# Kernel optimization log

Measured on AMD Instinct MI355X. Metric: run time of the kernel, lower is better.

The kernel has to match this reference:

```python
import jax, jax.numpy as jnp
import numpy as np

E = 8        # num_experts
TOPK = 2     # num_experts_per_tok
D = 1024     # n_embd
H = 2816     # grok FFN hidden dim (multiple_of-rounded 2/3*4*D)
B, T = 4, 2048
COEFF = 0.01 # moe_aux_loss_coeff


def setup_inputs() -> dict:
    key = jax.random.key(0)
    ks = jax.random.split(key, 8)
    s = 0.02  # weight scale so activations stay well-conditioned
    return {
        "x": jax.random.normal(ks[0], (B, T, D), jnp.float32),
        "gate_w": jax.random.normal(ks[1], (D, E), jnp.float32) * s,
        "expert_gate": jax.random.normal(ks[2], (E, D, H), jnp.float32) * s,
        "expert_up": jax.random.normal(ks[3], (E, D, H), jnp.float32) * s,
        "expert_down": jax.random.normal(ks[4], (E, H, D), jnp.float32) * s,
        "shared_gate": jax.random.normal(ks[5], (D, H), jnp.float32) * s,
        "shared_up": jax.random.normal(ks[6], (D, H), jnp.float32) * s,
        "shared_down": jax.random.normal(ks[7], (H, D), jnp.float32) * s,
    }


def _grok_ffn(x, g, u, d):
    # down(gelu(gate(x)) * up(x)); torch F.gelu default = exact erf gelu
    return (jax.nn.gelu(x @ g, approximate=False) * (x @ u)) @ d


def reference(x, gate_w, expert_gate, expert_up, expert_down,
              shared_gate, shared_up, shared_down):
    Bb, Tt, Dd = x.shape
    N = Bb * Tt
    xf = x.reshape(N, Dd)

    # --- router ---
    logits = (xf @ gate_w).astype(jnp.float32)            # (N, E)
    top_logits, top_idx = jax.lax.top_k(logits, TOPK)     # (N, K)
    top_w = jax.nn.softmax(top_logits, axis=-1)           # (N, K)
    gates = jax.nn.softmax(logits, axis=-1)               # (N, E)
    f = jnp.mean(jax.nn.one_hot(top_idx[:, 0], E, dtype=jnp.float32), axis=0)
    P = gates.mean(axis=0)
    aux_loss = COEFF * E * jnp.sum(f * P)

    # dense combine weights (N, E): 0 for unassigned experts
    comb = jnp.zeros((N, E), xf.dtype).at[
        jnp.arange(N)[:, None], top_idx].add(top_w.astype(xf.dtype))

    # --- experts: loop over small fixed E, weight-masked dense FFN ---
    out = jnp.zeros_like(xf)
    for e in range(E):
        ye = _grok_ffn(xf, expert_gate[e], expert_up[e], expert_down[e])
        out = out + comb[:, e:e + 1] * ye

    out = out.reshape(Bb, Tt, Dd)
    out = out + _grok_ffn(xf, shared_gate, shared_up, shared_down).reshape(Bb, Tt, Dd)
    return out, aux_loss
```

## Files before the change

### kernel.cpp

```cpp
#include <hip/hip_runtime.h>
#include <hip/hip_bf16.h>

#define NTOK 8192
#define DIM  1024
#define HID  2816
#define ROWS_CAP 25600
#define TCAP 200

typedef __bf16 bf16x8 __attribute__((ext_vector_type(8)));
typedef float  f32x4  __attribute__((ext_vector_type(4)));

__device__ __forceinline__ unsigned short f2bf(float f) {
  unsigned int x = __float_as_uint(f);
  unsigned int r = (x + 0x7fffu + ((x >> 16) & 1u)) >> 16;
  return (unsigned short)r;
}
__device__ __forceinline__ float gelu_erf(float g) {
  return 0.5f * g * (1.0f + erff(g * 0.70710678118654752f));
}

__device__ __forceinline__ void gload16(const void* g, void* l) {
  __builtin_amdgcn_global_load_lds(
      (__attribute__((address_space(1))) void*)(g),
      (__attribute__((address_space(3))) void*)(l), 16, 0, 0);
}

__device__ __forceinline__ void transpose64(const float* __restrict__ in,
                                            unsigned short* __restrict__ out,
                                            int R, int C) {
  __shared__ float t[64][65];
  int c0 = blockIdx.x * 64, r0 = blockIdx.y * 64;
  int tid = threadIdx.x;
  int lr = tid >> 4;
  int lc4 = (tid & 15) * 4;
  #pragma unroll
  for (int it = 0; it < 4; ++it) {
    int row = lr + it * 16;
    float4 v = *(const float4*)(in + (size_t)(r0 + row) * C + c0 + lc4);
    t[row][lc4] = v.x; t[row][lc4 + 1] = v.y;
    t[row][lc4 + 2] = v.z; t[row][lc4 + 3] = v.w;
  }
  __syncthreads();
  #pragma unroll
  for (int it = 0; it < 4; ++it) {
    int cloc = lr + it * 16;
    ushort4 w = make_ushort4(f2bf(t[lc4][cloc]), f2bf(t[lc4 + 1][cloc]),
                             f2bf(t[lc4 + 2][cloc]), f2bf(t[lc4 + 3][cloc]));
    *(ushort4*)(out + (size_t)(c0 + cloc) * R + r0 + lc4) = w;
  }
}

__global__ __launch_bounds__(256) void k_transpose_DH(
    const float* __restrict__ eg, const float* __restrict__ eu,
    const float* __restrict__ sg, const float* __restrict__ su,
    unsigned short* __restrict__ WgT, unsigned short* __restrict__ WuT,
    unsigned short* __restrict__ SgT, unsigned short* __restrict__ SuT) {
  int z = blockIdx.z;
  const float* in; unsigned short* out;
  if (z < 8)        { in = eg + (size_t)z * DIM * HID;       out = WgT + (size_t)z * DIM * HID; }
  else if (z < 16)  { in = eu + (size_t)(z - 8) * DIM * HID; out = WuT + (size_t)(z - 8) * DIM * HID; }
  else if (z == 16) { in = sg; out = SgT; }
  else              { in = su; out = SuT; }
  transpose64(in, out, DIM, HID);
}

__global__ __launch_bounds__(256) void k_transpose_HD(
    const float* __restrict__ ed, const float* __restrict__ sd,
    unsigned short* __restrict__ WdT, unsigned short* __restrict__ SdT) {
  int z = blockIdx.z;
  const float* in; unsigned short* out;
  if (z < 8) { in = ed + (size_t)z * HID * DIM; out = WdT + (size_t)z * HID * DIM; }
  else       { in = sd; out = SdT; }
  transpose64(in, out, HID, DIM);
}


__global__ __launch_bounds__(256) void k_router(const float* __restrict__ x,
                                                const float* __restrict__ gw,
                                                unsigned short* __restrict__ xb,
                                                int* __restrict__ top_idx,
                                                float* __restrict__ top_w,
                                                int* __restrict__ counts,
                                                float* __restrict__ f_cnt,
                                                float* __restrict__ P_sum) {
  __shared__ float s_p[8];
  __shared__ int   s_cnt[8];
  __shared__ int   s_f[8];
  int tid = threadIdx.x;
  if (tid < 8) { s_p[tid] = 0.f; s_cnt[tid] = 0; s_f[tid] = 0; }
  __syncthreads();

  int lane = tid & 63, wv = tid >> 6;
  float ploc[8] = {0,0,0,0,0,0,0,0};
  int   cloc[8] = {0,0,0,0,0,0,0,0};
  int   floc[8] = {0,0,0,0,0,0,0,0};

  for (int t = blockIdx.x * 4 + wv; t < NTOK; t += 2048) {
    const float4* xr = (const float4*)(x + (size_t)t * DIM) + lane * 4;
    float4 v0 = xr[0], v1 = xr[1], v2 = xr[2], v3 = xr[3];
    float xv[16] = {v0.x, v0.y, v0.z, v0.w, v1.x, v1.y, v1.z, v1.w,
                    v2.x, v2.y, v2.z, v2.w, v3.x, v3.y, v3.z, v3.w};
    ushort4* xw = (ushort4*)(xb + (size_t)t * DIM + lane * 16);
    #pragma unroll
    for (int q = 0; q < 4; ++q)
      xw[q] = make_ushort4(f2bf(xv[q * 4]), f2bf(xv[q * 4 + 1]),
                           f2bf(xv[q * 4 + 2]), f2bf(xv[q * 4 + 3]));
    float acc[8] = {0.f,0.f,0.f,0.f,0.f,0.f,0.f,0.f};
    #pragma unroll
    for (int i = 0; i < 16; ++i) {
      const float* g = gw + (size_t)(lane * 16 + i) * 8;
      #pragma unroll
      for (int e = 0; e < 8; ++e) acc[e] += xv[i] * g[e];
    }
    #pragma unroll
    for (int e = 0; e < 8; ++e) {
      #pragma unroll
      for (int off = 32; off > 0; off >>= 1)
        acc[e] += __shfl_xor(acc[e], off, 64);
    }
    if (lane == 0) {
      int i1 = 0; float l1 = acc[0];
      #pragma unroll
      for (int e = 1; e < 8; ++e) if (acc[e] > l1) { l1 = acc[e]; i1 = e; }
      int i2 = -1; float l2 = -3.0e38f;
      #pragma unroll
      for (int e = 0; e < 8; ++e) if (e != i1 && acc[e] > l2) { l2 = acc[e]; i2 = e; }
      float e2 = expf(l2 - l1);
      float inv12 = 1.0f / (1.0f + e2);
      top_idx[2 * t] = i1; top_idx[2 * t + 1] = i2;
      top_w[2 * t] = inv12; top_w[2 * t + 1] = e2 * inv12;
      float s = 0.f, p[8];
      #pragma unroll
      for (int e = 0; e < 8; ++e) { p[e] = expf(acc[e] - l1); s += p[e]; }
      float invs = 1.0f / s;
      #pragma unroll
      for (int e = 0; e < 8; ++e) {
        ploc[e] += p[e] * invs;
        cloc[e] += (e == i1) + (e == i2);
        floc[e] += (e == i1);
      }
    }
  }
  if (lane == 0) {
    #pragma unroll
    for (int e = 0; e < 8; ++e) {
      atomicAdd(&s_p[e], ploc[e]);
      atomicAdd(&s_cnt[e], cloc[e]);
      atomicAdd(&s_f[e], floc[e]);
    }
  }
  __syncthreads();
  if (tid < 8) {
    atomicAdd(&P_sum[tid], s_p[tid]);
    atomicAdd(&counts[tid], s_cnt[tid]);
    atomicAdd(&f_cnt[tid], (float)s_f[tid]);
  }
}


__global__ __launch_bounds__(256) void k_setup(const int* __restrict__ counts,
                                               int* __restrict__ cursors,
                                               int* __restrict__ tile_expert,
                                               int* __restrict__ tile_row0,
                                               int* __restrict__ perm,
                                               float* __restrict__ wrow) {
  int t = threadIdx.x;
  for (int r = t; r < ROWS_CAP; r += 256) {
    perm[r] = (r < NTOK) ? r : 0;
    wrow[r] = (r < NTOK) ? 1.0f : 0.0f;
  }
  if (t == 0) {
    int so[8], pe[8];
    int cur = NTOK;
    for (int e = 0; e < 8; ++e) {
      so[e] = cur;
      pe[e] = ((counts[e] + 127) >> 7) << 7;
      cur += pe[e];
    }
    for (int e = 0; e < 8; ++e) cursors[e] = so[e];
    for (int tile = 0; tile < TCAP; ++tile) {
      int r0 = tile << 7;
      int ex;
      if (tile < NTOK / 128) ex = 8;
      else if (r0 < cur) {
        ex = 0;
        for (int e = 0; e < 8; ++e) if (r0 >= so[e] && r0 < so[e] + pe[e]) ex = e;
      } else ex = -1;
      tile_expert[tile] = ex;
      tile_row0[tile] = r0;
    }
  }
}

__global__ __launch_bounds__(256) void k_scatter(const int* __restrict__ top_idx,
                                                 const float* __restrict__ top_w,
                                                 int* __restrict__ cursors,
                                                 int* __restrict__ perm,
                                                 float* __restrict__ wrow) {
  int i = blockIdx.x * 256 + threadIdx.x;
  if (i < NTOK * 2) {
    int e = top_idx[i];
    float w = top_w[i];
    int slot = atomicAdd(&cursors[e], 1);
    perm[slot] = i >> 1;
    wrow[slot] = w;
  }
}


__global__ __launch_bounds__(256) void k_stageA(const unsigned short* __restrict__ xb,
    const unsigned short* __restrict__ WgT, const unsigned short* __restrict__ WuT,
    const unsigned short* __restrict__ SgT, const unsigned short* __restrict__ SuT,
    const int* __restrict__ perm,
    const int* __restrict__ tile_expert, const int* __restrict__ tile_row0,
    unsigned short* __restrict__ h, int t0, int row_base) {
  int tile = t0 + blockIdx.y;
  int e = tile_expert[tile];
  if (e < 0) return;
  const unsigned short* Bg = (e < 8) ? WgT + (size_t)e * HID * DIM : SgT;
  const unsigned short* Bu = (e < 8) ? WuT + (size_t)e * HID * DIM : SuT;
  int rows0 = tile_row0[tile];
  int h0 = blockIdx.x * 64;

  __shared__ unsigned short As[2][128 * 64];
  __shared__ unsigned short Bgs[2][64 * 64];
  __shared__ unsigned short Bus[2][64 * 64];

  int tid = threadIdx.x, lane = tid & 63, wv = tid >> 6;
  int wr = wv >> 1, wc = wv & 1;
  int rlo = lane >> 3;
  int koff = (((lane & 7) ^ rlo) * 8);
  int rsw = (lane & 7) << 4;

  int prow[4];
  #pragma unroll
  for (int i = 0; i < 4; ++i) prow[i] = perm[rows0 + i * 32 + wv * 8 + rlo];
  int bn[2];
  #pragma unroll
  for (int i = 0; i < 2; ++i) bn[i] = h0 + i * 32 + wv * 8 + rlo;

  f32x4 accg[4][2] = {};
  f32x4 accu[4][2] = {};

  auto stage = [&](int b, int k0) {
    #pragma unroll
    for (int i = 0; i < 4; ++i)
      gload16(xb + (size_t)prow[i] * DIM + k0 + koff, (char*)As[b] + (i * 32 + wv * 8) * 128);
    #pragma unroll
    for (int i = 0; i < 2; ++i) {
      gload16(Bg + (size_t)bn[i] * DIM + k0 + koff, (char*)Bgs[b] + (i * 32 + wv * 8) * 128);
      gload16(Bu + (size_t)bn[i] * DIM + k0 + koff, (char*)Bus[b] + (i * 32 + wv * 8) * 128);
    }
  };

  auto compute = [&](int b) {
    #pragma unroll
    for (int kk = 0; kk < 2; ++kk) {
      int kbyte = (kk * 64 + (lane >> 4) * 16) ^ rsw;
      bf16x8 a[4], bg[2], bu[2];
      #pragma unroll
      for (int mi = 0; mi < 4; ++mi)
        a[mi] = *(const bf16x8*)((const char*)As[b] + (wr * 64 + mi * 16 + (lane & 15)) * 128 + kbyte);
      #pragma unroll
      for (int ni = 0; ni < 2; ++ni) {
        bg[ni] = *(const bf16x8*)((const char*)Bgs[b] + (wc * 32 + ni * 16 + (lane & 15)) * 128 + kbyte);
        bu[ni] = *(const bf16x8*)((const char*)Bus[b] + (wc * 32 + ni * 16 + (lane & 15)) * 128 + kbyte);
      }
      #pragma unroll
      for (int mi = 0; mi < 4; ++mi) {
        #pragma unroll
        for (int ni = 0; ni < 2; ++ni) {
          accg[mi][ni] = __builtin_amdgcn_mfma_f32_16x16x32_bf16(a[mi], bg[ni], accg[mi][ni], 0, 0, 0);
          accu[mi][ni] = __builtin_amdgcn_mfma_f32_16x16x32_bf16(a[mi], bu[ni], accu[mi][ni], 0, 0, 0);
        }
      }
    }
  };

  stage(0, 0);
  int cur = 0;
  for (int kb = 0; kb < DIM / 64 - 1; ++kb) {
    stage(cur ^ 1, (kb + 1) * 64);
    __builtin_amdgcn_sched_barrier(0);
    asm volatile("s_waitcnt vmcnt(6)" ::: "memory");
    __builtin_amdgcn_s_barrier();
    __builtin_amdgcn_sched_barrier(0);
    __builtin_amdgcn_s_setprio(1);
    compute(cur);
    __builtin_amdgcn_s_setprio(0);
    __builtin_amdgcn_s_barrier();
    cur ^= 1;
  }
  asm volatile("s_waitcnt vmcnt(0)" ::: "memory");
  __builtin_amdgcn_s_barrier();
  __builtin_amdgcn_sched_barrier(0);
  compute(cur);

  #pragma unroll
  for (int mi = 0; mi < 4; ++mi) {
    #pragma unroll
    for (int ni = 0; ni < 2; ++ni) {
      #pragma unroll
      for (int j = 0; j < 4; ++j) {
        int rg = rows0 - row_base + wr * 64 + mi * 16 + (lane >> 4) * 4 + j;
        int cg = h0 + wc * 32 + ni * 16 + (lane & 15);
        float g = accg[mi][ni][j];
        float u = accu[mi][ni][j];
        h[(size_t)rg * HID + cg] = f2bf(gelu_erf(g) * u);
      }
    }
  }
}


template <bool STORE>
__global__ __launch_bounds__(256) void k_stageB(const unsigned short* __restrict__ h,
    const unsigned short* __restrict__ WdT, const unsigned short* __restrict__ SdT,
    const int* __restrict__ perm, const float* __restrict__ wrow,
    const int* __restrict__ tile_expert, const int* __restrict__ tile_row0,
    float* __restrict__ out, int t0, int row_base) {
  int tile = t0 + blockIdx.y;
  int e = tile_expert[tile];
  if (e < 0) return;
  const unsigned short* Bd = (e < 8) ? WdT + (size_t)e * DIM * HID : SdT;
  int rows0 = tile_row0[tile];
  int n0 = blockIdx.x * 128;

  __shared__ unsigned short As[2][128 * 64];
  __shared__ unsigned short Bs[2][128 * 64];

  int tid = threadIdx.x, lane = tid & 63, wv = tid >> 6;
  int wr = wv >> 1, wc = wv & 1;
  int rlo = lane >> 3;
  int koff = (((lane & 7) ^ rlo) * 8);
  int rsw = (lane & 7) << 4;

  f32x4 acc[4][4] = {};

  auto stage = [&](int b, int k0) {
    #pragma unroll
    for (int i = 0; i < 4; ++i) {
      int rb = i * 32 + wv * 8;
      int r = rb + rlo;
      gload16(h + (size_t)(rows0 - row_base + r) * HID + k0 + koff, (char*)As[b] + rb * 128);
      gload16(Bd + (size_t)(n0 + r) * HID + k0 + koff, (char*)Bs[b] + rb * 128);
    }
  };

  auto compute = [&](int b) {
    #pragma unroll
    for (int kk = 0; kk < 2; ++kk) {
      int kbyte = (kk * 64 + (lane >> 4) * 16) ^ rsw;
      bf16x8 a[4], bb[4];
      #pragma unroll
      for (int mi = 0; mi < 4; ++mi)
        a[mi] = *(const bf16x8*)((const char*)As[b] + (wr * 64 + mi * 16 + (lane & 15)) * 128 + kbyte);
      #pragma unroll
      for (int ni = 0; ni < 4; ++ni)
        bb[ni] = *(const bf16x8*)((const char*)Bs[b] + (wc * 64 + ni * 16 + (lane & 15)) * 128 + kbyte);
      #pragma unroll
      for (int mi = 0; mi < 4; ++mi) {
        #pragma unroll
        for (int ni = 0; ni < 4; ++ni)
          acc[mi][ni] = __builtin_amdgcn_mfma_f32_16x16x32_bf16(a[mi], bb[ni], acc[mi][ni], 0, 0, 0);
      }
    }
  };

  stage(0, 0);
  int cur = 0;
  for (int kb = 0; kb < HID / 64 - 1; ++kb) {
    stage(cur ^ 1, (kb + 1) * 64);
    __builtin_amdgcn_sched_barrier(0);
    asm volatile("s_waitcnt vmcnt(8)" ::: "memory");
    __builtin_amdgcn_s_barrier();
    __builtin_amdgcn_sched_barrier(0);
    __builtin_amdgcn_s_setprio(1);
    compute(cur);
    __builtin_amdgcn_s_setprio(0);
    __builtin_amdgcn_s_barrier();
    cur ^= 1;
  }
  asm volatile("s_waitcnt vmcnt(0)" ::: "memory");
  __builtin_amdgcn_s_barrier();
  __builtin_amdgcn_sched_barrier(0);
  compute(cur);

  #pragma unroll
  for (int mi = 0; mi < 4; ++mi) {
    #pragma unroll
    for (int j = 0; j < 4; ++j) {
      int rl = wr * 64 + mi * 16 + (lane >> 4) * 4 + j;
      int token = perm[rows0 + rl];
      float w = wrow[rows0 + rl];
      #pragma unroll
      for (int ni = 0; ni < 4; ++ni) {
        int col = n0 + wc * 64 + ni * 16 + (lane & 15);
        if (STORE) out[(size_t)token * DIM + col] = w * acc[mi][ni][j];
        else atomicAdd(&out[(size_t)token * DIM + col], w * acc[mi][ni][j]);
      }
    }
  }
}


__global__ void k_aux(const float* __restrict__ f_cnt, const float* __restrict__ P_sum,
                      float* __restrict__ aux_out) {
  if (threadIdx.x == 0 && blockIdx.x == 0) {
    float a = 0.f;
    #pragma unroll
    for (int e = 0; e < 8; ++e) a += f_cnt[e] * P_sum[e];
    a *= 0.01f * 8.f / ((float)NTOK * (float)NTOK);
    aux_out[0] = a;
  }
}


extern "C" void kernel_launch(void* const* d_in, const int* in_sizes, int n_in,
                              void* d_out, int out_size, void* d_ws, size_t ws_size,
                              hipStream_t stream) {
  const float* x  = (const float*)d_in[0];
  const float* gw = (const float*)d_in[1];
  const float* eg = (const float*)d_in[2];
  const float* eu = (const float*)d_in[3];
  const float* ed = (const float*)d_in[4];
  const float* sg = (const float*)d_in[5];
  const float* su = (const float*)d_in[6];
  const float* sd = (const float*)d_in[7];
  float* out = (float*)d_out;

  char* ws = (char*)d_ws;
  size_t off = 0;
  auto take = [&](size_t sz) { size_t o = off; off += (sz + 255) & ~(size_t)255; return o; };
  const size_t OFF_XB   = take((size_t)NTOK * DIM * 2);
  const size_t OFF_WGT  = take((size_t)8 * HID * DIM * 2);
  const size_t OFF_WUT  = take((size_t)8 * HID * DIM * 2);
  const size_t OFF_WDT  = take((size_t)8 * HID * DIM * 2);
  const size_t OFF_SGT  = take((size_t)HID * DIM * 2);
  const size_t OFF_SUT  = take((size_t)HID * DIM * 2);
  const size_t OFF_SDT  = take((size_t)HID * DIM * 2);
  const size_t OFF_TI   = take((size_t)NTOK * 2 * 4);
  const size_t OFF_TW   = take((size_t)NTOK * 2 * 4);
  const size_t OFF_PERM = take((size_t)ROWS_CAP * 4);
  const size_t OFF_WROW = take((size_t)ROWS_CAP * 4);
  const size_t OFF_STATS= take(256);
  const size_t OFF_CURS = take(256);
  const size_t OFF_TE   = take(TCAP * 4);
  const size_t OFF_TR   = take(TCAP * 4);
  const size_t OFF_H    = off;

  const size_t TILE_H_BYTES = (size_t)128 * HID * 2;
  size_t avail = (ws_size > OFF_H) ? (ws_size - OFF_H) : 0;
  int G = (int)((avail / TILE_H_BYTES < (size_t)TCAP) ? (avail / TILE_H_BYTES) : (size_t)TCAP);
  if (G < 1) return;

  unsigned short* xb  = (unsigned short*)(ws + OFF_XB);
  unsigned short* WgT = (unsigned short*)(ws + OFF_WGT);
  unsigned short* WuT = (unsigned short*)(ws + OFF_WUT);
  unsigned short* WdT = (unsigned short*)(ws + OFF_WDT);
  unsigned short* SgT = (unsigned short*)(ws + OFF_SGT);
  unsigned short* SuT = (unsigned short*)(ws + OFF_SUT);
  unsigned short* SdT = (unsigned short*)(ws + OFF_SDT);
  int* top_idx        = (int*)(ws + OFF_TI);
  float* top_w        = (float*)(ws + OFF_TW);
  int* perm           = (int*)(ws + OFF_PERM);
  float* wrow         = (float*)(ws + OFF_WROW);
  int* counts         = (int*)(ws + OFF_STATS);
  float* f_cnt        = (float*)(ws + OFF_STATS + 32);
  float* P_sum        = (float*)(ws + OFF_STATS + 64);
  int* cursors        = (int*)(ws + OFF_CURS);
  int* tile_expert    = (int*)(ws + OFF_TE);
  int* tile_row0      = (int*)(ws + OFF_TR);
  unsigned short* hbuf = (unsigned short*)(ws + OFF_H);

  hipMemsetAsync(ws + OFF_STATS, 0, 256, stream);

  k_transpose_DH<<<dim3(HID / 64, DIM / 64, 18), 256, 0, stream>>>(
      eg, eu, sg, su, WgT, WuT, SgT, SuT);
  k_transpose_HD<<<dim3(DIM / 64, HID / 64, 9), 256, 0, stream>>>(
      ed, sd, WdT, SdT);

  k_router<<<512, 256, 0, stream>>>(x, gw, xb, top_idx, top_w, counts, f_cnt, P_sum);
  k_setup<<<1, 256, 0, stream>>>(counts, cursors, tile_expert, tile_row0, perm, wrow);
  k_scatter<<<NTOK * 2 / 256, 256, 0, stream>>>(top_idx, top_w, cursors, perm, wrow);

  for (int t0 = 0; t0 < TCAP; t0 += G) {
    int nt = (TCAP - t0 < G) ? (TCAP - t0) : G;
    int row_base = t0 * 128;
    k_stageA<<<dim3(HID / 64, nt), 256, 0, stream>>>(xb, WgT, WuT, SgT, SuT, perm,
                                                     tile_expert, tile_row0, hbuf, t0, row_base);
    int ns = 0;
    if (t0 < 64) { ns = 64 - t0; if (ns > nt) ns = nt; }
    int ne = nt - ns;
    if (ns > 0)
      k_stageB<true><<<dim3(DIM / 128, ns), 256, 0, stream>>>(hbuf, WdT, SdT, perm, wrow,
                                                              tile_expert, tile_row0, out, t0, row_base);
    if (ne > 0)
      k_stageB<false><<<dim3(DIM / 128, ne), 256, 0, stream>>>(hbuf, WdT, SdT, perm, wrow,
                                                               tile_expert, tile_row0, out, t0 + ns, row_base);
  }

  k_aux<<<1, 64, 0, stream>>>(f_cnt, P_sum, out + (size_t)NTOK * DIM);
}
```

Baseline: 922.8 us.

## Interleave gate/up weights and enlarge stage-A tiles to 256x256 with 512 threads

Gate and up projection weights are transposed into one interleaved matrix in 16-column groups, so stage A runs a single GEMM whose N tile holds matched gate and up columns. The stage-A tile grows from 128 rows x 64 hidden to 256 rows x 256 interleaved columns using 512 threads and 8x4 MFMA accumulators per wave. This raises arithmetic intensity and operand reuse per LDS load. Expert padding rises to multiples of 256 rows, which adds wasted compute, and the larger per-wave register and LDS footprint (128KB) may reduce occupancy.

```diff
diff --git a/kernel.cpp b/kernel.cpp
--- a/kernel.cpp
+++ b/kernel.cpp
@@ -4,8 +4,10 @@
 #define NTOK 8192
 #define DIM  1024
 #define HID  2816
-#define ROWS_CAP 25600
-#define TCAP 200
+#define NI   (2 * HID)
+#define ROWS_CAP 26880
+#define TC256 104
+#define TC128 208
 
 typedef __bf16 bf16x8 __attribute__((ext_vector_type(8)));
 typedef float  f32x4  __attribute__((ext_vector_type(4)));
@@ -27,7 +29,7 @@
 
 __device__ __forceinline__ void transpose64(const float* __restrict__ in,
                                             unsigned short* __restrict__ out,
-                                            int R, int C) {
+                                            int R, int C, int iloff) {
   __shared__ float t[64][65];
   int c0 = blockIdx.x * 64, r0 = blockIdx.y * 64;
   int tid = threadIdx.x;
@@ -44,24 +46,25 @@
   #pragma unroll
   for (int it = 0; it < 4; ++it) {
     int cloc = lr + it * 16;
+    int c = c0 + cloc;
+    int rowil = (iloff < 0) ? c : (((c >> 4) << 5) + (c & 15) + iloff);
     ushort4 w = make_ushort4(f2bf(t[lc4][cloc]), f2bf(t[lc4 + 1][cloc]),
                              f2bf(t[lc4 + 2][cloc]), f2bf(t[lc4 + 3][cloc]));
-    *(ushort4*)(out + (size_t)(c0 + cloc) * R + r0 + lc4) = w;
+    *(ushort4*)(out + (size_t)rowil * R + r0 + lc4) = w;
   }
 }
 
 __global__ __launch_bounds__(256) void k_transpose_DH(
     const float* __restrict__ eg, const float* __restrict__ eu,
     const float* __restrict__ sg, const float* __restrict__ su,
-    unsigned short* __restrict__ WgT, unsigned short* __restrict__ WuT,
-    unsigned short* __restrict__ SgT, unsigned short* __restrict__ SuT) {
+    unsigned short* __restrict__ WI, unsigned short* __restrict__ SI) {
   int z = blockIdx.z;
-  const float* in; unsigned short* out;
-  if (z < 8)        { in = eg + (size_t)z * DIM * HID;       out = WgT + (size_t)z * DIM * HID; }
-  else if (z < 16)  { in = eu + (size_t)(z - 8) * DIM * HID; out = WuT + (size_t)(z - 8) * DIM * HID; }
-  else if (z == 16) { in = sg; out = SgT; }
-  else              { in = su; out = SuT; }
-  transpose64(in, out, DIM, HID);
+  const float* in; unsigned short* out; int off;
+  if (z < 8)        { in = eg + (size_t)z * DIM * HID;       out = WI + (size_t)z * NI * DIM; off = 0; }
+  else if (z < 16)  { in = eu + (size_t)(z - 8) * DIM * HID; out = WI + (size_t)(z - 8) * NI * DIM; off = 16; }
+  else if (z == 16) { in = sg; out = SI; off = 0; }
+  else              { in = su; out = SI; off = 16; }
+  transpose64(in, out, DIM, HID, off);
 }
 
 __global__ __launch_bounds__(256) void k_transpose_HD(
@@ -71,7 +74,7 @@
   const float* in; unsigned short* out;
   if (z < 8) { in = ed + (size_t)z * HID * DIM; out = WdT + (size_t)z * HID * DIM; }
   else       { in = sd; out = SdT; }
-  transpose64(in, out, HID, DIM);
+  transpose64(in, out, HID, DIM, -1);
 }
 
 
@@ -160,8 +163,8 @@
 
 __global__ __launch_bounds__(256) void k_setup(const int* __restrict__ counts,
                                                int* __restrict__ cursors,
-                                               int* __restrict__ tile_expert,
-                                               int* __restrict__ tile_row0,
+                                               int* __restrict__ te256,
+                                               int* __restrict__ te128,
                                                int* __restrict__ perm,
                                                float* __restrict__ wrow) {
   int t = threadIdx.x;
@@ -174,20 +177,29 @@
     int cur = NTOK;
     for (int e = 0; e < 8; ++e) {
       so[e] = cur;
-      pe[e] = ((counts[e] + 127) >> 7) << 7;
+      pe[e] = ((counts[e] + 255) >> 8) << 8;
       cur += pe[e];
     }
     for (int e = 0; e < 8; ++e) cursors[e] = so[e];
-    for (int tile = 0; tile < TCAP; ++tile) {
-      int r0 = tile << 7;
+    for (int T = 0; T < TC256; ++T) {
+      int r0 = T << 8;
       int ex;
-      if (tile < NTOK / 128) ex = 8;
+      if (T < NTOK / 256) ex = 8;
       else if (r0 < cur) {
         ex = 0;
         for (int e = 0; e < 8; ++e) if (r0 >= so[e] && r0 < so[e] + pe[e]) ex = e;
       } else ex = -1;
-      tile_expert[tile] = ex;
-      tile_row0[tile] = r0;
+      te256[T] = ex;
+    }
+    for (int ht = 0; ht < TC128; ++ht) {
+      int r0 = ht << 7;
+      int ex;
+      if (ht < NTOK / 128) ex = 8;
+      else if (r0 < cur) {
+        ex = 0;
+        for (int e = 0; e < 8; ++e) if (r0 >= so[e] && r0 < so[e] + pe[e]) ex = e;
+      } else ex = -1;
+      te128[ht] = ex;
     }
   }
 }
@@ -208,71 +220,61 @@
 }
 
 
-__global__ __launch_bounds__(256) void k_stageA(const unsigned short* __restrict__ xb,
-    const unsigned short* __restrict__ WgT, const unsigned short* __restrict__ WuT,
-    const unsigned short* __restrict__ SgT, const unsigned short* __restrict__ SuT,
-    const int* __restrict__ perm,
-    const int* __restrict__ tile_expert, const int* __restrict__ tile_row0,
-    unsigned short* __restrict__ h, int t0, int row_base) {
-  int tile = t0 + blockIdx.y;
-  int e = tile_expert[tile];
+__global__ __launch_bounds__(512) void k_stageA(const unsigned short* __restrict__ xb,
+    const unsigned short* __restrict__ WI, const unsigned short* __restrict__ SI,
+    const int* __restrict__ perm, const int* __restrict__ te256,
+    unsigned short* __restrict__ h, int T0, int row_base) {
+  int T = T0 + blockIdx.y;
+  int e = te256[T];
   if (e < 0) return;
-  const unsigned short* Bg = (e < 8) ? WgT + (size_t)e * HID * DIM : SgT;
-  const unsigned short* Bu = (e < 8) ? WuT + (size_t)e * HID * DIM : SuT;
-  int rows0 = tile_row0[tile];
-  int h0 = blockIdx.x * 64;
-
-  __shared__ unsigned short As[2][128 * 64];
-  __shared__ unsigned short Bgs[2][64 * 64];
-  __shared__ unsigned short Bus[2][64 * 64];
-
-  int tid = threadIdx.x, lane = tid & 63, wv = tid >> 6;
-  int wr = wv >> 1, wc = wv & 1;
+  const unsigned short* B = (e < 8) ? WI + (size_t)e * NI * DIM : SI;
+  int rows0 = T * 256;
+  int c0i = blockIdx.x * 256;
+
+  __shared__ unsigned short As[2][256 * 64];
+  __shared__ unsigned short Bs[2][256 * 64];
+
+  int tid = threadIdx.x, lane = tid & 63, w = tid >> 6;
+  int wr = w >> 2, wc = w & 3;
   int rlo = lane >> 3;
-  int koff = (((lane & 7) ^ rlo) * 8);
-  int rsw = (lane & 7) << 4;
+  int koff = ((lane & 7) ^ rlo) * 8;
+  int fr = lane & 15;
 
   int prow[4];
   #pragma unroll
-  for (int i = 0; i < 4; ++i) prow[i] = perm[rows0 + i * 32 + wv * 8 + rlo];
-  int bn[2];
+  for (int i = 0; i < 4; ++i) prow[i] = perm[rows0 + i * 64 + w * 8 + rlo];
+  const unsigned short* bsrc[4];
   #pragma unroll
-  for (int i = 0; i < 2; ++i) bn[i] = h0 + i * 32 + wv * 8 + rlo;
-
-  f32x4 accg[4][2] = {};
-  f32x4 accu[4][2] = {};
+  for (int i = 0; i < 4; ++i)
+    bsrc[i] = B + (size_t)(c0i + i * 64 + w * 8 + rlo) * DIM + koff;
+
+  f32x4 acc[8][4] = {};
 
   auto stage = [&](int b, int k0) {
     #pragma unroll
     for (int i = 0; i < 4; ++i)
-      gload16(xb + (size_t)prow[i] * DIM + k0 + koff, (char*)As[b] + (i * 32 + wv * 8) * 128);
-    #pragma unroll
-    for (int i = 0; i < 2; ++i) {
-      gload16(Bg + (size_t)bn[i] * DIM + k0 + koff, (char*)Bgs[b] + (i * 32 + wv * 8) * 128);
-      gload16(Bu + (size_t)bn[i] * DIM + k0 + koff, (char*)Bus[b] + (i * 32 + wv * 8) * 128);
-    }
+      gload16(xb + (size_t)prow[i] * DIM + k0 + koff, (char*)As[b] + (i * 64 + w * 8) * 128);
+    #pragma unroll
+    for (int i = 0; i < 4; ++i)
+      gload16(bsrc[i] + k0, (char*)Bs[b] + (i * 64 + w * 8) * 128);
   };
 
   auto compute = [&](int b) {
     #pragma unroll
     for (int kk = 0; kk < 2; ++kk) {
-      int kbyte = (kk * 64 + (lane >> 4) * 16) ^ rsw;
-      bf16x8 a[4], bg[2], bu[2];
-      #pragma unroll
-      for (int mi = 0; mi < 4; ++mi)
-        a[mi] = *(const bf16x8*)((const char*)As[b] + (wr * 64 + mi * 16 + (lane & 15)) * 128 + kbyte);
-      #pragma unroll
-      for (int ni = 0; ni < 2; ++ni) {
-        bg[ni] = *(const bf16x8*)((const char*)Bgs[b] + (wc * 32 + ni * 16 + (lane & 15)) * 128 + kbyte);
-        bu[ni] = *(const bf16x8*)((const char*)Bus[b] + (wc * 32 + ni * 16 + (lane & 15)) * 128 + kbyte);
-      }
-      #pragma unroll
-      for (int mi = 0; mi < 4; ++mi) {
+      int kbyte = (kk * 64 + (lane >> 4) * 16) ^ ((lane & 7) << 4);
+      bf16x8 a[8], bf[4];
+      #pragma unroll
+      for (int mi = 0; mi < 8; ++mi)
+        a[mi] = *(const bf16x8*)((const char*)As[b] + (wr * 128 + mi * 16 + fr) * 128 + kbyte);
+      #pragma unroll
+      for (int ni = 0; ni < 4; ++ni)
+        bf[ni] = *(const bf16x8*)((const char*)Bs[b] + (wc * 64 + ni * 16 + fr) * 128 + kbyte);
+      #pragma unroll
+      for (int mi = 0; mi < 8; ++mi) {
         #pragma unroll
-        for (int ni = 0; ni < 2; ++ni) {
-          accg[mi][ni] = __builtin_amdgcn_mfma_f32_16x16x32_bf16(a[mi], bg[ni], accg[mi][ni], 0, 0, 0);
-          accu[mi][ni] = __builtin_amdgcn_mfma_f32_16x16x32_bf16(a[mi], bu[ni], accu[mi][ni], 0, 0, 0);
-        }
+        for (int ni = 0; ni < 4; ++ni)
+          acc[mi][ni] = __builtin_amdgcn_mfma_f32_16x16x32_bf16(a[mi], bf[ni], acc[mi][ni], 0, 0, 0);
       }
     }
   };
@@ -282,7 +284,7 @@
   for (int kb = 0; kb < DIM / 64 - 1; ++kb) {
     stage(cur ^ 1, (kb + 1) * 64);
     __builtin_amdgcn_sched_barrier(0);
-    asm volatile("s_waitcnt vmcnt(6)" ::: "memory");
+    asm volatile("s_waitcnt vmcnt(8)" ::: "memory");
     __builtin_amdgcn_s_barrier();
     __builtin_amdgcn_sched_barrier(0);
     __builtin_amdgcn_s_setprio(1);
@@ -297,15 +299,15 @@
   compute(cur);
 
   #pragma unroll
-  for (int mi = 0; mi < 4; ++mi) {
-    #pragma unroll
-    for (int ni = 0; ni < 2; ++ni) {
+  for (int mi = 0; mi < 8; ++mi) {
+    #pragma unroll
+    for (int p = 0; p < 2; ++p) {
       #pragma unroll
       for (int j = 0; j < 4; ++j) {
-        int rg = rows0 - row_base + wr * 64 + mi * 16 + (lane >> 4) * 4 + j;
-        int cg = h0 + wc * 32 + ni * 16 + (lane & 15);
-        float g = accg[mi][ni][j];
-        float u = accu[mi][ni][j];
+        int rg = rows0 - row_base + wr * 128 + mi * 16 + (lane >> 4) * 4 + j;
+        int cg = blockIdx.x * 128 + wc * 32 + p * 16 + fr;
+        float g = acc[mi][2 * p][j];
+        float u = acc[mi][2 * p + 1][j];
         h[(size_t)rg * HID + cg] = f2bf(gelu_erf(g) * u);
       }
     }
@@ -317,13 +319,13 @@
 __global__ __launch_bounds__(256) void k_stageB(const unsigned short* __restrict__ h,
     const unsigned short* __restrict__ WdT, const unsigned short* __restrict__ SdT,
     const int* __restrict__ perm, const float* __restrict__ wrow,
-    const int* __restrict__ tile_expert, const int* __restrict__ tile_row0,
+    const int* __restrict__ te128,
     float* __restrict__ out, int t0, int row_base) {
   int tile = t0 + blockIdx.y;
-  int e = tile_expert[tile];
+  int e = te128[tile];
   if (e < 0) return;
   const unsigned short* Bd = (e < 8) ? WdT + (size_t)e * DIM * HID : SdT;
-  int rows0 = tile_row0[tile];
+  int rows0 = tile * 128;
   int n0 = blockIdx.x * 128;
 
   __shared__ unsigned short As[2][128 * 64];
@@ -433,11 +435,9 @@
   size_t off = 0;
   auto take = [&](size_t sz) { size_t o = off; off += (sz + 255) & ~(size_t)255; return o; };
   const size_t OFF_XB   = take((size_t)NTOK * DIM * 2);
-  const size_t OFF_WGT  = take((size_t)8 * HID * DIM * 2);
-  const size_t OFF_WUT  = take((size_t)8 * HID * DIM * 2);
+  const size_t OFF_WI   = take((size_t)8 * NI * DIM * 2);
+  const size_t OFF_SI   = take((size_t)NI * DIM * 2);
   const size_t OFF_WDT  = take((size_t)8 * HID * DIM * 2);
-  const size_t OFF_SGT  = take((size_t)HID * DIM * 2);
-  const size_t OFF_SUT  = take((size_t)HID * DIM * 2);
   const size_t OFF_SDT  = take((size_t)HID * DIM * 2);
   const size_t OFF_TI   = take((size_t)NTOK * 2 * 4);
   const size_t OFF_TW   = take((size_t)NTOK * 2 * 4);
@@ -445,21 +445,19 @@
   const size_t OFF_WROW = take((size_t)ROWS_CAP * 4);
   const size_t OFF_STATS= take(256);
   const size_t OFF_CURS = take(256);
-  const size_t OFF_TE   = take(TCAP * 4);
-  const size_t OFF_TR   = take(TCAP * 4);
+  const size_t OFF_TE2  = take(TC256 * 4);
+  const size_t OFF_TE1  = take(TC128 * 4);
   const size_t OFF_H    = off;
 
-  const size_t TILE_H_BYTES = (size_t)128 * HID * 2;
+  const size_t TILE_H_BYTES = (size_t)256 * HID * 2;
   size_t avail = (ws_size > OFF_H) ? (ws_size - OFF_H) : 0;
-  int G = (int)((avail / TILE_H_BYTES < (size_t)TCAP) ? (avail / TILE_H_BYTES) : (size_t)TCAP);
+  int G = (int)((avail / TILE_H_BYTES < (size_t)TC256) ? (avail / TILE_H_BYTES) : (size_t)TC256);
   if (G < 1) return;
 
   unsigned short* xb  = (unsigned short*)(ws + OFF_XB);
-  unsigned short* WgT = (unsigned short*)(ws + OFF_WGT);
-  unsigned short* WuT = (unsigned short*)(ws + OFF_WUT);
+  unsigned short* WI  = (unsigned short*)(ws + OFF_WI);
+  unsigned short* SI  = (unsigned short*)(ws + OFF_SI);
   unsigned short* WdT = (unsigned short*)(ws + OFF_WDT);
-  unsigned short* SgT = (unsigned short*)(ws + OFF_SGT);
-  unsigned short* SuT = (unsigned short*)(ws + OFF_SUT);
   unsigned short* SdT = (unsigned short*)(ws + OFF_SDT);
   int* top_idx        = (int*)(ws + OFF_TI);
   float* top_w        = (float*)(ws + OFF_TW);
@@ -469,35 +467,36 @@
   float* f_cnt        = (float*)(ws + OFF_STATS + 32);
   float* P_sum        = (float*)(ws + OFF_STATS + 64);
   int* cursors        = (int*)(ws + OFF_CURS);
-  int* tile_expert    = (int*)(ws + OFF_TE);
-  int* tile_row0      = (int*)(ws + OFF_TR);
+  int* te256          = (int*)(ws + OFF_TE2);
+  int* te128          = (int*)(ws + OFF_TE1);
   unsigned short* hbuf = (unsigned short*)(ws + OFF_H);
 
   hipMemsetAsync(ws + OFF_STATS, 0, 256, stream);
 
   k_transpose_DH<<<dim3(HID / 64, DIM / 64, 18), 256, 0, stream>>>(
-      eg, eu, sg, su, WgT, WuT, SgT, SuT);
+      eg, eu, sg, su, WI, SI);
   k_transpose_HD<<<dim3(DIM / 64, HID / 64, 9), 256, 0, stream>>>(
       ed, sd, WdT, SdT);
 
   k_router<<<512, 256, 0, stream>>>(x, gw, xb, top_idx, top_w, counts, f_cnt, P_sum);
-  k_setup<<<1, 256, 0, stream>>>(counts, cursors, tile_expert, tile_row0, perm, wrow);
+  k_setup<<<1, 256, 0, stream>>>(counts, cursors, te256, te128, perm, wrow);
   k_scatter<<<NTOK * 2 / 256, 256, 0, stream>>>(top_idx, top_w, cursors, perm, wrow);
 
-  for (int t0 = 0; t0 < TCAP; t0 += G) {
-    int nt = (TCAP - t0 < G) ? (TCAP - t0) : G;
-    int row_base = t0 * 128;
-    k_stageA<<<dim3(HID / 64, nt), 256, 0, stream>>>(xb, WgT, WuT, SgT, SuT, perm,
-                                                     tile_expert, tile_row0, hbuf, t0, row_base);
+  for (int T0 = 0; T0 < TC256; T0 += G) {
+    int nt = (TC256 - T0 < G) ? (TC256 - T0) : G;
+    int row_base = T0 * 256;
+    k_stageA<<<dim3(NI / 256, nt), 512, 0, stream>>>(xb, WI, SI, perm, te256,
+                                                     hbuf, T0, row_base);
+    int h0t = T0 * 2, hn = nt * 2;
     int ns = 0;
-    if (t0 < 64) { ns = 64 - t0; if (ns > nt) ns = nt; }
-    int ne = nt - ns;
+    if (h0t < 64) { ns = 64 - h0t; if (ns > hn) ns = hn; }
+    int ne = hn - ns;
     if (ns > 0)
       k_stageB<true><<<dim3(DIM / 128, ns), 256, 0, stream>>>(hbuf, WdT, SdT, perm, wrow,
-                                                              tile_expert, tile_row0, out, t0, row_base);
+                                                              te128, out, h0t, row_base);
     if (ne > 0)
       k_stageB<false><<<dim3(DIM / 128, ne), 256, 0, stream>>>(hbuf, WdT, SdT, perm, wrow,
-                                                               tile_expert, tile_row0, out, t0 + ns, row_base);
+                                                               te128, out, h0t + ns, row_base);
   }
 
   k_aux<<<1, 64, 0, stream>>>(f_cnt, P_sum, out + (size_t)NTOK * DIM);
```

Result: no change. 925.2 us (+0.3%).
